# Kernel tuning notes

Hardware: AMD Instinct MI355X
Metric: run time of the kernel (lower is better)

## Reference

```python
import jax, jax.numpy as jnp
import numpy as np

N_NODES = 100000
N_EDGES = 1_600_000
F_IN = 500   # PubMed num_node_features
HID = 128
N_CLASSES = 3


def _glorot(key, shape):
    fan_in, fan_out = shape
    limit = np.sqrt(6.0 / (fan_in + fan_out)).astype(np.float32)
    return jax.random.uniform(key, shape, jnp.float32, -limit, limit)


def setup_inputs() -> dict:
    key = jax.random.key(0)
    ks = jax.random.split(key, 8)
    x = jax.random.normal(ks[0], (N_NODES, F_IN), jnp.float32)
    edge_index = jax.random.randint(ks[1], (2, N_EDGES), 0, N_NODES, jnp.int64)
    dims = [(F_IN, HID), (HID, HID), (HID, HID), (HID, HID), (HID, N_CLASSES)]
    inp = {"x": x, "edge_index": edge_index}
    for i, d in enumerate(dims):
        inp[f"W{i+1}"] = _glorot(ks[2 + i], d)
        inp[f"b{i+1}"] = jnp.zeros((d[1],), jnp.float32)
    return inp


def _gcn_conv(h, W, b, src, dst, norm, n):
    # linear transform then normalized neighbor aggregation (scatter-add)
    h = h @ W                                   # [N, out]
    msg = h[src] * norm                         # gather along edges, [E+N, out]
    return jax.ops.segment_sum(msg, dst, num_segments=n) + b


def reference(x, edge_index, W1, b1, W2, b2, W3, b3, W4, b4, W5, b5):
    n = x.shape[0]
    loops = jnp.arange(n)
    src = jnp.concatenate([edge_index[0], loops])  # add self-loops (PyG default)
    dst = jnp.concatenate([edge_index[1], loops])
    # symmetric normalization: deg^{-1/2}[dst] * deg^{-1/2}[src], deg over self-looped graph
    deg = jax.ops.segment_sum(jnp.ones_like(dst, x.dtype), dst, num_segments=n)
    dis = jnp.where(deg > 0, jax.lax.rsqrt(jnp.maximum(deg, 1e-12)), 0.0)
    norm = (dis[src] * dis[dst])[:, None]

    h = jax.nn.relu(_gcn_conv(x, W1, b1, src, dst, norm, n))
    # dropout p=0.5 is identity in eval mode
    h = jax.nn.relu(_gcn_conv(h, W2, b2, src, dst, norm, n))
    h = jax.nn.relu(_gcn_conv(h, W3, b3, src, dst, norm, n))
    h = jax.nn.relu(_gcn_conv(h, W4, b4, src, dst, norm, n))
    return _gcn_conv(h, W5, b5, src, dst, norm, n)
```

## Files before the change

kernel.cpp:

```cpp
#include <hip/hip_runtime.h>
#include <hip/hip_bf16.h>

#define NN 100000
#define NNP 100096
#define NE 1600000
#define FIN 500
#define HID 128

typedef __attribute__((ext_vector_type(8))) short short8;
typedef __attribute__((ext_vector_type(4))) float f32x4;

__device__ __forceinline__ float bf2f(unsigned short u) {
    return __uint_as_float(((unsigned int)u) << 16);
}
__device__ __forceinline__ unsigned short f2bf(float f) {
    __hip_bfloat16 h = __float2bfloat16(f);
    return *(unsigned short*)&h;
}
__device__ __forceinline__ float lo16(unsigned int v) { return __uint_as_float(v << 16); }
__device__ __forceinline__ float hi16(unsigned int v) { return __uint_as_float(v & 0xffff0000u); }


__global__ __launch_bounds__(256) void GCNLarge_20761871909627_kernel(int* __restrict__ buf, int n) {
    int i = blockIdx.x * 256 + threadIdx.x;
    if (i < n) buf[i] = 0;
}


__global__ void detect_kernel(const int* __restrict__ ei, const unsigned int* __restrict__ xw,
                              int* __restrict__ flags) {
    int lane = threadIdx.x & 63;
    int any = 0;
    for (int k = lane; k < 128; k += 64) any |= ei[2 * k + 1];
    int hits = 0;
    for (int k = lane; k < 256; k += 64) {
        unsigned e = (xw[k] >> 7) & 0xFF;
        hits += (e >= 100 && e <= 140) ? 1 : 0;
    }
#pragma unroll
    for (int o = 32; o > 0; o >>= 1) {
        any |= __shfl_down(any, o);
        hits += __shfl_down(hits, o);
    }
    if (lane == 0) {
        flags[0] = (any == 0) ? 1 : 0;
        flags[1] = (hits >= 128) ? 1 : 0;
    }
}

__device__ __forceinline__ int edge_src(const int* ei, int e, int m) {
    return m ? ei[2 * (size_t)e] : ei[e];
}
__device__ __forceinline__ int edge_dst(const int* ei, int e, int m) {
    return m ? ei[2 * (size_t)NE + 2 * (size_t)e] : ei[(size_t)NE + e];
}


__global__ __launch_bounds__(256) void count_kernel(const int* __restrict__ ei,
                                                    const int* __restrict__ flags,
                                                    int* __restrict__ cnt) {
    int e = blockIdx.x * 256 + threadIdx.x;
    if (e < NE) {
        int d = edge_dst(ei, e, flags[0]);
        if ((unsigned)d < NN) atomicAdd(&cnt[d], 1);
    }
}

__global__ __launch_bounds__(256) void dis_kernel(const int* __restrict__ cnt,
                                                  float* __restrict__ dis) {
    int i = blockIdx.x * 256 + threadIdx.x;
    if (i < NNP) {
        int c = (i < NN) ? cnt[i] : 0;
        if (c < 0) c = 0;
        dis[i] = rsqrtf((float)(c + 1));
    }
}

__global__ __launch_bounds__(1024) void scan1_kernel(const int* __restrict__ cnt,
                                                     int* __restrict__ off,
                                                     int* __restrict__ bsum) {
    __shared__ int s[1024];
    int i = blockIdx.x * 1024 + threadIdx.x;
    int v = (i < NN) ? cnt[i] : 0;
    s[threadIdx.x] = v;
    __syncthreads();
    for (int d = 1; d < 1024; d <<= 1) {
        int tv = (threadIdx.x >= d) ? s[threadIdx.x - d] : 0;
        __syncthreads();
        s[threadIdx.x] += tv;
        __syncthreads();
    }
    if (i < NN) off[i] = s[threadIdx.x] - v;
    if (threadIdx.x == 1023) bsum[blockIdx.x] = s[1023];
}

__global__ void scan2_kernel(int* __restrict__ bsum, int nb) {
    if (threadIdx.x == 0 && blockIdx.x == 0) {
        int acc = 0;
        for (int b = 0; b < nb; b++) { int v = bsum[b]; bsum[b] = acc; acc += v; }
    }
}

__global__ __launch_bounds__(1024) void scan3_kernel(int* __restrict__ off,
                                                     const int* __restrict__ bsum,
                                                     int* __restrict__ cursor) {
    int i = blockIdx.x * 1024 + threadIdx.x;
    if (i < NN) { int o = off[i] + bsum[blockIdx.x]; off[i] = o; cursor[i] = o; }
    if (i == 0) off[NN] = NE;
}

__global__ __launch_bounds__(256) void place_kernel(const int* __restrict__ ei,
                                                    const int* __restrict__ flags,
                                                    int* __restrict__ cursor,
                                                    int* __restrict__ csr) {
    int e = blockIdx.x * 256 + threadIdx.x;
    if (e < NE) {
        int m = flags[0];
        int s = edge_src(ei, e, m);
        int d = edge_dst(ei, e, m);
        if ((unsigned)s < NN && (unsigned)d < NN) {
            int slot = atomicAdd(&cursor[d], 1);
            if ((unsigned)slot < NE) csr[slot] = s;
        }
    }
}


__global__ __launch_bounds__(256) void wt_kernel(const void* __restrict__ W,
                                                 const int* __restrict__ flags,
                                                 unsigned short* __restrict__ Wt,
                                                 int K, int Kpad, int total) {
    int idx = blockIdx.x * 256 + threadIdx.x;
    if (idx >= total) return;
    int n = idx / Kpad, k = idx - n * Kpad;
    unsigned short v = 0;
    if (k < K) {
        if (flags[1]) v = ((const unsigned short*)W)[(size_t)k * HID + n];
        else          v = f2bf(((const float*)W)[(size_t)k * HID + n]);
    }
    Wt[idx] = v;
}


__global__ __launch_bounds__(256) void gemmWr_kernel(const unsigned short* __restrict__ A,
                                                     const unsigned short* __restrict__ Wt,
                                                     const float* __restrict__ dis,
                                                     unsigned short* __restrict__ out) {
    int tid = threadIdx.x;
    int w = tid >> 6, lane = tid & 63;
    int m = lane & 15, quad = lane >> 4;
    int mbase = (w >> 1) * 32, nbase = (w & 1) * 64;
    short8 b[4][4];
#pragma unroll
    for (int nt = 0; nt < 4; nt++)
#pragma unroll
        for (int kq = 0; kq < 4; kq++)
            b[nt][kq] = *(const short8*)(Wt + (size_t)(nbase + nt * 16 + m) * HID + kq * 32 + quad * 8);
    int t0 = blockIdx.x * 4;
    short8 aP[4][2], aQ[4][2];
    auto loadA = [&](int t, short8 a[4][2]) {
        const unsigned short* p0 = A + (size_t)(t * 64 + mbase + m) * HID + quad * 8;
        const unsigned short* p1 = p0 + (size_t)16 * HID;
#pragma unroll
        for (int kq = 0; kq < 4; kq++) {
            a[kq][0] = *(const short8*)(p0 + kq * 32);
            a[kq][1] = *(const short8*)(p1 + kq * 32);
        }
    };
    loadA(t0, aP);
#pragma unroll
    for (int tt = 0; tt < 4; tt++) {
        if (tt < 3) loadA(t0 + tt + 1, (tt & 1) ? aP : aQ);
        short8 (*ac)[2] = (tt & 1) ? aQ : aP;
        f32x4 acc[2][4] = {};
#pragma unroll
        for (int kq = 0; kq < 4; kq++)
#pragma unroll
            for (int nt = 0; nt < 4; nt++) {
                acc[0][nt] = __builtin_amdgcn_mfma_f32_16x16x32_bf16(ac[kq][0], b[nt][kq], acc[0][nt], 0, 0, 0);
                acc[1][nt] = __builtin_amdgcn_mfma_f32_16x16x32_bf16(ac[kq][1], b[nt][kq], acc[1][nt], 0, 0, 0);
            }
        int r0 = (t0 + tt) * 64;
#pragma unroll
        for (int mt = 0; mt < 2; mt++) {
            int rb = r0 + mbase + mt * 16 + quad * 4;
#pragma unroll
            for (int reg = 0; reg < 4; reg++) {
                float d = dis[rb + reg];
#pragma unroll
                for (int nt = 0; nt < 4; nt++)
                    out[(size_t)(rb + reg) * HID + nbase + nt * 16 + m] = f2bf(acc[mt][nt][reg] * d);
            }
        }
    }
}


__global__ __launch_bounds__(256) void gemm1r_kernel(const void* __restrict__ Av,
                                                     const unsigned short* __restrict__ Wt1,
                                                     const float* __restrict__ dis,
                                                     const int* __restrict__ flags,
                                                     unsigned short* __restrict__ out) {
    int tid = threadIdx.x;
    int bf = flags[1];
    int w = tid >> 6, lane = tid & 63;
    int m = lane & 15, quad = lane >> 4;
    int mbase = (w >> 1) * 32, nbase = (w & 1) * 64;
    int r0 = blockIdx.x * 64;
    int row0 = r0 + mbase + m;       int rc0 = (row0 < NN) ? row0 : NN - 1;
    int row1 = r0 + mbase + 16 + m;  int rc1 = (row1 < NN) ? row1 : NN - 1;
    f32x4 acc[2][4] = {};
#pragma unroll
    for (int kc = 0; kc < 4; kc++) {
        short8 b[4][4];
#pragma unroll
        for (int nt = 0; nt < 4; nt++)
#pragma unroll
            for (int kq = 0; kq < 4; kq++)
                b[nt][kq] = *(const short8*)(Wt1 + (size_t)(nbase + nt * 16 + m) * 512 + kc * 128 + kq * 32 + quad * 8);
        short8 a[4][2];
#pragma unroll
        for (int kq = 0; kq < 4; kq++) {
            int k_off = kc * 128 + kq * 32 + quad * 8;
            ushort4 z = make_ushort4(0, 0, 0, 0);
#pragma unroll
            for (int mt = 0; mt < 2; mt++) {
                int rr = mt ? rc1 : rc0;
                ushort4 lo = z, hi = z;
                if (bf) {
                    const unsigned short* xp = (const unsigned short*)Av + (size_t)rr * FIN + k_off;
                    if (k_off + 4 <= FIN) lo = *(const ushort4*)xp;
                    if (k_off + 8 <= FIN) hi = *(const ushort4*)(xp + 4);
                } else {
                    const float* xp = (const float*)Av + (size_t)rr * FIN + k_off;
                    if (k_off + 4 <= FIN) { float4 f = *(const float4*)xp;
                        lo = make_ushort4(f2bf(f.x), f2bf(f.y), f2bf(f.z), f2bf(f.w)); }
                    if (k_off + 8 <= FIN) { float4 f = *(const float4*)(xp + 4);
                        hi = make_ushort4(f2bf(f.x), f2bf(f.y), f2bf(f.z), f2bf(f.w)); }
                }
                a[kq][mt] = short8{(short)lo.x, (short)lo.y, (short)lo.z, (short)lo.w,
                                   (short)hi.x, (short)hi.y, (short)hi.z, (short)hi.w};
            }
        }
#pragma unroll
        for (int kq = 0; kq < 4; kq++)
#pragma unroll
            for (int nt = 0; nt < 4; nt++) {
                acc[0][nt] = __builtin_amdgcn_mfma_f32_16x16x32_bf16(a[kq][0], b[nt][kq], acc[0][nt], 0, 0, 0);
                acc[1][nt] = __builtin_amdgcn_mfma_f32_16x16x32_bf16(a[kq][1], b[nt][kq], acc[1][nt], 0, 0, 0);
            }
    }
#pragma unroll
    for (int mt = 0; mt < 2; mt++) {
        int rb = r0 + mbase + mt * 16 + quad * 4;
#pragma unroll
        for (int reg = 0; reg < 4; reg++) {
            int row = rb + reg;
            if (row < NN) {
                float d = dis[row];
#pragma unroll
                for (int nt = 0; nt < 4; nt++)
                    out[(size_t)row * HID + nbase + nt * 16 + m] = f2bf(acc[mt][nt][reg] * d);
            }
        }
    }
}


__global__ __launch_bounds__(256) void aggb_kernel(const unsigned short* __restrict__ tin,
                                                   const int* __restrict__ off,
                                                   const int* __restrict__ csr,
                                                   const float* __restrict__ dis,
                                                   const void* __restrict__ bias,
                                                   const int* __restrict__ flags,
                                                   unsigned short* __restrict__ hout,
                                                   int relu, int scale_src) {
    int node = blockIdx.x * 4 + (threadIdx.x >> 6);
    int lane = threadIdx.x & 63;
    float di = dis[node];
    unsigned int sv = *(const unsigned int*)(tin + (size_t)node * HID + lane * 2);
    float acc0 = scale_src ? di * lo16(sv) : lo16(sv);
    float acc1 = scale_src ? di * hi16(sv) : hi16(sv);
    int e0 = off[node], e1 = off[node + 1];
    if (e0 < 0) e0 = 0;
    if (e1 > NE) e1 = NE;
    int e = e0;
    if (!scale_src) {
        for (; e + 8 <= e1; e += 8) {
            int i0 = csr[e],     i1 = csr[e + 1], i2 = csr[e + 2], i3 = csr[e + 3];
            int i4 = csr[e + 4], i5 = csr[e + 5], i6 = csr[e + 6], i7 = csr[e + 7];
            unsigned int v0 = *(const unsigned int*)(tin + (size_t)i0 * HID + lane * 2);
            unsigned int v1 = *(const unsigned int*)(tin + (size_t)i1 * HID + lane * 2);
            unsigned int v2 = *(const unsigned int*)(tin + (size_t)i2 * HID + lane * 2);
            unsigned int v3 = *(const unsigned int*)(tin + (size_t)i3 * HID + lane * 2);
            unsigned int v4 = *(const unsigned int*)(tin + (size_t)i4 * HID + lane * 2);
            unsigned int v5 = *(const unsigned int*)(tin + (size_t)i5 * HID + lane * 2);
            unsigned int v6 = *(const unsigned int*)(tin + (size_t)i6 * HID + lane * 2);
            unsigned int v7 = *(const unsigned int*)(tin + (size_t)i7 * HID + lane * 2);
            acc0 += lo16(v0); acc1 += hi16(v0); acc0 += lo16(v1); acc1 += hi16(v1);
            acc0 += lo16(v2); acc1 += hi16(v2); acc0 += lo16(v3); acc1 += hi16(v3);
            acc0 += lo16(v4); acc1 += hi16(v4); acc0 += lo16(v5); acc1 += hi16(v5);
            acc0 += lo16(v6); acc1 += hi16(v6); acc0 += lo16(v7); acc1 += hi16(v7);
        }
        for (; e + 4 <= e1; e += 4) {
            int i0 = csr[e], i1 = csr[e + 1], i2 = csr[e + 2], i3 = csr[e + 3];
            unsigned int v0 = *(const unsigned int*)(tin + (size_t)i0 * HID + lane * 2);
            unsigned int v1 = *(const unsigned int*)(tin + (size_t)i1 * HID + lane * 2);
            unsigned int v2 = *(const unsigned int*)(tin + (size_t)i2 * HID + lane * 2);
            unsigned int v3 = *(const unsigned int*)(tin + (size_t)i3 * HID + lane * 2);
            acc0 += lo16(v0); acc1 += hi16(v0); acc0 += lo16(v1); acc1 += hi16(v1);
            acc0 += lo16(v2); acc1 += hi16(v2); acc0 += lo16(v3); acc1 += hi16(v3);
        }
        for (; e < e1; e++) {
            int s = csr[e];
            unsigned int v = *(const unsigned int*)(tin + (size_t)s * HID + lane * 2);
            acc0 += lo16(v); acc1 += hi16(v);
        }
    } else {
        for (; e + 8 <= e1; e += 8) {
            int i0 = csr[e],     i1 = csr[e + 1], i2 = csr[e + 2], i3 = csr[e + 3];
            int i4 = csr[e + 4], i5 = csr[e + 5], i6 = csr[e + 6], i7 = csr[e + 7];
            unsigned int v0 = *(const unsigned int*)(tin + (size_t)i0 * HID + lane * 2);
            unsigned int v1 = *(const unsigned int*)(tin + (size_t)i1 * HID + lane * 2);
            unsigned int v2 = *(const unsigned int*)(tin + (size_t)i2 * HID + lane * 2);
            unsigned int v3 = *(const unsigned int*)(tin + (size_t)i3 * HID + lane * 2);
            unsigned int v4 = *(const unsigned int*)(tin + (size_t)i4 * HID + lane * 2);
            unsigned int v5 = *(const unsigned int*)(tin + (size_t)i5 * HID + lane * 2);
            unsigned int v6 = *(const unsigned int*)(tin + (size_t)i6 * HID + lane * 2);
            unsigned int v7 = *(const unsigned int*)(tin + (size_t)i7 * HID + lane * 2);
            float m0 = dis[i0], m1 = dis[i1], m2 = dis[i2], m3 = dis[i3];
            float m4 = dis[i4], m5 = dis[i5], m6 = dis[i6], m7 = dis[i7];
            acc0 += m0 * lo16(v0); acc1 += m0 * hi16(v0);
            acc0 += m1 * lo16(v1); acc1 += m1 * hi16(v1);
            acc0 += m2 * lo16(v2); acc1 += m2 * hi16(v2);
            acc0 += m3 * lo16(v3); acc1 += m3 * hi16(v3);
            acc0 += m4 * lo16(v4); acc1 += m4 * hi16(v4);
            acc0 += m5 * lo16(v5); acc1 += m5 * hi16(v5);
            acc0 += m6 * lo16(v6); acc1 += m6 * hi16(v6);
            acc0 += m7 * lo16(v7); acc1 += m7 * hi16(v7);
        }
        for (; e < e1; e++) {
            int s = csr[e];
            unsigned int v = *(const unsigned int*)(tin + (size_t)s * HID + lane * 2);
            float mm = dis[s];
            acc0 += mm * lo16(v); acc1 += mm * hi16(v);
        }
    }
    float o0 = di * acc0, o1 = di * acc1;
    if (bias) {
        if (flags[1]) { o0 += bf2f(((const unsigned short*)bias)[lane * 2]);
                        o1 += bf2f(((const unsigned short*)bias)[lane * 2 + 1]); }
        else          { o0 += ((const float*)bias)[lane * 2];
                        o1 += ((const float*)bias)[lane * 2 + 1]; }
    }
    if (relu) { o0 = fmaxf(o0, 0.f); o1 = fmaxf(o1, 0.f); }
    unsigned int pk = ((unsigned int)f2bf(o1) << 16) | (unsigned int)f2bf(o0);
    *(unsigned int*)(hout + (size_t)node * HID + lane * 2) = pk;
}


__global__ __launch_bounds__(256) void gemm5_kernel(const unsigned short* __restrict__ A,
                                                    const void* __restrict__ W5v,
                                                    const void* __restrict__ b5v,
                                                    const int* __restrict__ flags,
                                                    void* __restrict__ outv) {
    __shared__ float Ws[384];
    __shared__ float bs[3];
    int tid = threadIdx.x;
    int bf = flags[1];
    for (int idx = tid; idx < 384; idx += 256)
        Ws[idx] = bf ? bf2f(((const unsigned short*)W5v)[idx]) : ((const float*)W5v)[idx];
    if (tid < 3)
        bs[tid] = bf ? bf2f(((const unsigned short*)b5v)[tid]) : ((const float*)b5v)[tid];
    __syncthreads();
    int lane = tid & 63;
    int row = blockIdx.x * 4 + (tid >> 6);
    float a0 = bf2f(A[(size_t)row * HID + lane]);
    float a1 = bf2f(A[(size_t)row * HID + 64 + lane]);
    float c0 = a0 * Ws[lane * 3 + 0] + a1 * Ws[(lane + 64) * 3 + 0];
    float c1 = a0 * Ws[lane * 3 + 1] + a1 * Ws[(lane + 64) * 3 + 1];
    float c2 = a0 * Ws[lane * 3 + 2] + a1 * Ws[(lane + 64) * 3 + 2];
#pragma unroll
    for (int o = 32; o > 0; o >>= 1) {
        c0 += __shfl_down(c0, o);
        c1 += __shfl_down(c1, o);
        c2 += __shfl_down(c2, o);
    }
    if (lane == 0) {
        c0 += bs[0]; c1 += bs[1]; c2 += bs[2];
        if (bf) {
            unsigned short* out = (unsigned short*)outv;
            out[(size_t)row * 3 + 0] = f2bf(c0);
            out[(size_t)row * 3 + 1] = f2bf(c1);
            out[(size_t)row * 3 + 2] = f2bf(c2);
        } else {
            float* out = (float*)outv;
            out[(size_t)row * 3 + 0] = c0;
            out[(size_t)row * 3 + 1] = c1;
            out[(size_t)row * 3 + 2] = c2;
        }
    }
}

extern "C" void kernel_launch(void* const* d_in, const int* in_sizes, int n_in,
                              void* d_out, int out_size, void* d_ws, size_t ws_size,
                              hipStream_t stream) {
    const void* x = nullptr; const int* ei = nullptr;
    const void* W1 = nullptr; const void* W5 = nullptr; const void* b5 = nullptr;
    const void* Wmid[3] = {nullptr, nullptr, nullptr};
    const void* bvec[4] = {nullptr, nullptr, nullptr, nullptr};
    int nw = 0, nb = 0;
    for (int i = 0; i < n_in; i++) {
        int s = in_sizes[i];
        if      (s == 50000000) x = d_in[i];
        else if (s == 3200000)  ei = (const int*)d_in[i];
        else if (s == 64000)    W1 = d_in[i];
        else if (s == 16384)  { if (nw < 3) Wmid[nw++] = d_in[i]; }
        else if (s == 384)      W5 = d_in[i];
        else if (s == 128)    { if (nb < 4) bvec[nb++] = d_in[i]; }
        else if (s == 3)        b5 = d_in[i];
    }
    if (!x || !ei || !W1 || !W5 || !b5 || nw < 3 || nb < 4) return;

    char* p = (char*)d_ws;
    auto alloc = [&](size_t bytes) { char* q = p; p += (bytes + 255) & ~(size_t)255; return (void*)q; };
    int*   flags = (int*)alloc(256);
    float* dis   = (float*)alloc((size_t)NNP * 4);
    int*   cnt   = (int*)alloc((size_t)NN * 4);
    int*   off   = (int*)alloc((size_t)(NN + 1) * 4);
    int*   cur   = (int*)alloc((size_t)NN * 4);
    int*   bsum  = (int*)alloc(128 * 4);
    int*   csr   = (int*)alloc((size_t)NE * 4);
    unsigned short* Wt1 = (unsigned short*)alloc((size_t)128 * 512 * 2);
    unsigned short* Wt2 = (unsigned short*)alloc((size_t)128 * 128 * 2);
    unsigned short* Wt3 = (unsigned short*)alloc((size_t)128 * 128 * 2);
    unsigned short* Wt4 = (unsigned short*)alloc((size_t)128 * 128 * 2);
    unsigned short* T   = (unsigned short*)alloc((size_t)NNP * HID * 2);
    unsigned short* H   = (unsigned short*)alloc((size_t)NNP * HID * 2);

    GCNLarge_20761871909627_kernel<<<(NN + 255) / 256, 256, 0, stream>>>(cnt, NN);
    detect_kernel<<<1, 64, 0, stream>>>(ei, (const unsigned int*)x, flags);
    wt_kernel<<<256, 256, 0, stream>>>(W1, flags, Wt1, FIN, 512, 128 * 512);
    wt_kernel<<<64, 256, 0, stream>>>(Wmid[0], flags, Wt2, HID, 128, 128 * 128);
    wt_kernel<<<64, 256, 0, stream>>>(Wmid[1], flags, Wt3, HID, 128, 128 * 128);
    wt_kernel<<<64, 256, 0, stream>>>(Wmid[2], flags, Wt4, HID, 128, 128 * 128);
    count_kernel<<<(NE + 255) / 256, 256, 0, stream>>>(ei, flags, cnt);
    dis_kernel<<<(NNP + 255) / 256, 256, 0, stream>>>(cnt, dis);
    scan1_kernel<<<98, 1024, 0, stream>>>(cnt, off, bsum);
    scan2_kernel<<<1, 64, 0, stream>>>(bsum, 98);
    scan3_kernel<<<98, 1024, 0, stream>>>(off, bsum, cur);
    place_kernel<<<(NE + 255) / 256, 256, 0, stream>>>(ei, flags, cur, csr);

    gemm1r_kernel<<<NNP / 64, 256, 0, stream>>>(x, Wt1, dis, flags, T);
    aggb_kernel<<<NN / 4, 256, 0, stream>>>(T, off, csr, dis, bvec[0], flags, H, 1, 0);
    gemmWr_kernel<<<NNP / 256, 256, 0, stream>>>(H, Wt2, dis, T);
    aggb_kernel<<<NN / 4, 256, 0, stream>>>(T, off, csr, dis, bvec[1], flags, H, 1, 0);
    gemmWr_kernel<<<NNP / 256, 256, 0, stream>>>(H, Wt3, dis, T);
    aggb_kernel<<<NN / 4, 256, 0, stream>>>(T, off, csr, dis, bvec[2], flags, H, 1, 0);
    gemmWr_kernel<<<NNP / 256, 256, 0, stream>>>(H, Wt4, dis, T);
    aggb_kernel<<<NN / 4, 256, 0, stream>>>(T, off, csr, dis, bvec[3], flags, H, 1, 0);
    aggb_kernel<<<NN / 4, 256, 0, stream>>>(H, off, csr, dis, nullptr, flags, T, 0, 1);
    gemm5_kernel<<<NN / 4, 256, 0, stream>>>(T, W5, b5, flags, d_out);
}
```

Measured before the change: 1.003 ms.

## Stage layer-1 GEMM through LDS, split aggregation wave into two edge halves, shrink GEMM tiles

```diff
diff --git a/kernel.cpp b/kernel.cpp
--- a/kernel.cpp
+++ b/kernel.cpp
@@ -6,6 +6,7 @@
 #define NE 1600000
 #define FIN 500
 #define HID 128
+#define LDK 136
 
 typedef __attribute__((ext_vector_type(8))) short short8;
 typedef __attribute__((ext_vector_type(4))) float f32x4;
@@ -142,7 +143,7 @@
 }
 
 
-__global__ __launch_bounds__(256) void gemmWr_kernel(const unsigned short* __restrict__ A,
+__global__ __launch_bounds__(256) void gemmW1_kernel(const unsigned short* __restrict__ A,
                                                      const unsigned short* __restrict__ Wt,
                                                      const float* __restrict__ dis,
                                                      unsigned short* __restrict__ out) {
@@ -150,66 +151,106 @@
     int w = tid >> 6, lane = tid & 63;
     int m = lane & 15, quad = lane >> 4;
     int mbase = (w >> 1) * 32, nbase = (w & 1) * 64;
+    int r0 = blockIdx.x * 64;
     short8 b[4][4];
 #pragma unroll
     for (int nt = 0; nt < 4; nt++)
 #pragma unroll
         for (int kq = 0; kq < 4; kq++)
             b[nt][kq] = *(const short8*)(Wt + (size_t)(nbase + nt * 16 + m) * HID + kq * 32 + quad * 8);
-    int t0 = blockIdx.x * 4;
-    short8 aP[4][2], aQ[4][2];
-    auto loadA = [&](int t, short8 a[4][2]) {
-        const unsigned short* p0 = A + (size_t)(t * 64 + mbase + m) * HID + quad * 8;
+    short8 a[4][2];
+    {
+        const unsigned short* p0 = A + (size_t)(r0 + mbase + m) * HID + quad * 8;
         const unsigned short* p1 = p0 + (size_t)16 * HID;
 #pragma unroll
         for (int kq = 0; kq < 4; kq++) {
             a[kq][0] = *(const short8*)(p0 + kq * 32);
             a[kq][1] = *(const short8*)(p1 + kq * 32);
         }
-    };
-    loadA(t0, aP);
-#pragma unroll
-    for (int tt = 0; tt < 4; tt++) {
-        if (tt < 3) loadA(t0 + tt + 1, (tt & 1) ? aP : aQ);
-        short8 (*ac)[2] = (tt & 1) ? aQ : aP;
-        f32x4 acc[2][4] = {};
-#pragma unroll
-        for (int kq = 0; kq < 4; kq++)
-#pragma unroll
-            for (int nt = 0; nt < 4; nt++) {
-                acc[0][nt] = __builtin_amdgcn_mfma_f32_16x16x32_bf16(ac[kq][0], b[nt][kq], acc[0][nt], 0, 0, 0);
-                acc[1][nt] = __builtin_amdgcn_mfma_f32_16x16x32_bf16(ac[kq][1], b[nt][kq], acc[1][nt], 0, 0, 0);
-            }
-        int r0 = (t0 + tt) * 64;
-#pragma unroll
-        for (int mt = 0; mt < 2; mt++) {
-            int rb = r0 + mbase + mt * 16 + quad * 4;
-#pragma unroll
-            for (int reg = 0; reg < 4; reg++) {
-                float d = dis[rb + reg];
-#pragma unroll
-                for (int nt = 0; nt < 4; nt++)
-                    out[(size_t)(rb + reg) * HID + nbase + nt * 16 + m] = f2bf(acc[mt][nt][reg] * d);
-            }
-        }
-    }
-}
-
-
-__global__ __launch_bounds__(256) void gemm1r_kernel(const void* __restrict__ Av,
-                                                     const unsigned short* __restrict__ Wt1,
-                                                     const float* __restrict__ dis,
-                                                     const int* __restrict__ flags,
-                                                     unsigned short* __restrict__ out) {
+    }
+    f32x4 acc[2][4] = {};
+#pragma unroll
+    for (int kq = 0; kq < 4; kq++)
+#pragma unroll
+        for (int nt = 0; nt < 4; nt++) {
+            acc[0][nt] = __builtin_amdgcn_mfma_f32_16x16x32_bf16(a[kq][0], b[nt][kq], acc[0][nt], 0, 0, 0);
+            acc[1][nt] = __builtin_amdgcn_mfma_f32_16x16x32_bf16(a[kq][1], b[nt][kq], acc[1][nt], 0, 0, 0);
+        }
+#pragma unroll
+    for (int mt = 0; mt < 2; mt++) {
+        int rb = r0 + mbase + mt * 16 + quad * 4;
+#pragma unroll
+        for (int reg = 0; reg < 4; reg++) {
+            float d = dis[rb + reg];
+#pragma unroll
+            for (int nt = 0; nt < 4; nt++)
+                out[(size_t)(rb + reg) * HID + nbase + nt * 16 + m] = f2bf(acc[mt][nt][reg] * d);
+        }
+    }
+}
+
+
+__global__ __launch_bounds__(256, 3) void gemm1d_kernel(const void* __restrict__ Av,
+                                                        const unsigned short* __restrict__ Wt1,
+                                                        const float* __restrict__ dis,
+                                                        const int* __restrict__ flags,
+                                                        unsigned short* __restrict__ out) {
+    __shared__ unsigned short As[2][64 * LDK];
     int tid = threadIdx.x;
     int bf = flags[1];
+    int r0 = blockIdx.x * 64;
     int w = tid >> 6, lane = tid & 63;
     int m = lane & 15, quad = lane >> 4;
     int mbase = (w >> 1) * 32, nbase = (w & 1) * 64;
-    int r0 = blockIdx.x * 64;
-    int row0 = r0 + mbase + m;       int rc0 = (row0 < NN) ? row0 : NN - 1;
-    int row1 = r0 + mbase + 16 + m;  int rc1 = (row1 < NN) ? row1 : NN - 1;
     f32x4 acc[2][4] = {};
+    short8 s[4];
+
+    auto stage = [&](int kc) {
+#pragma unroll
+        for (int i = 0; i < 4; i++) {
+            int idx = tid + i * 256;
+            int r = idx >> 4, c = idx & 15;
+            int row = r0 + r; if (row >= NN) row = NN - 1;
+            int kk = kc * 128 + c * 8;
+            short8 p = {};
+            if (bf) {
+                const unsigned short* xp = (const unsigned short*)Av + (size_t)row * FIN + kk;
+                if (kk + 8 <= FIN) {
+                    ushort4 lo = *(const ushort4*)xp;
+                    ushort4 hi = *(const ushort4*)(xp + 4);
+                    p = short8{(short)lo.x, (short)lo.y, (short)lo.z, (short)lo.w,
+                               (short)hi.x, (short)hi.y, (short)hi.z, (short)hi.w};
+                } else if (kk + 4 <= FIN) {
+                    ushort4 lo = *(const ushort4*)xp;
+                    p = short8{(short)lo.x, (short)lo.y, (short)lo.z, (short)lo.w, 0, 0, 0, 0};
+                }
+            } else {
+                const float* xp = (const float*)Av + (size_t)row * FIN + kk;
+                if (kk + 8 <= FIN) {
+                    float4 f0 = *(const float4*)xp;
+                    float4 f1 = *(const float4*)(xp + 4);
+                    p = short8{(short)f2bf(f0.x), (short)f2bf(f0.y), (short)f2bf(f0.z), (short)f2bf(f0.w),
+                               (short)f2bf(f1.x), (short)f2bf(f1.y), (short)f2bf(f1.z), (short)f2bf(f1.w)};
+                } else if (kk + 4 <= FIN) {
+                    float4 f0 = *(const float4*)xp;
+                    p = short8{(short)f2bf(f0.x), (short)f2bf(f0.y), (short)f2bf(f0.z), (short)f2bf(f0.w),
+                               0, 0, 0, 0};
+                }
+            }
+            s[i] = p;
+        }
+    };
+    auto wrlds = [&](int buf) {
+#pragma unroll
+        for (int i = 0; i < 4; i++) {
+            int idx = tid + i * 256;
+            int r = idx >> 4, c = idx & 15;
+            *(short8*)&As[buf][r * LDK + c * 8] = s[i];
+        }
+    };
+
+    stage(0);
+    wrlds(0);
 #pragma unroll
     for (int kc = 0; kc < 4; kc++) {
         short8 b[4][4];
@@ -218,37 +259,20 @@
 #pragma unroll
             for (int kq = 0; kq < 4; kq++)
                 b[nt][kq] = *(const short8*)(Wt1 + (size_t)(nbase + nt * 16 + m) * 512 + kc * 128 + kq * 32 + quad * 8);
-        short8 a[4][2];
+        __syncthreads();
+        if (kc < 3) stage(kc + 1);
+        const unsigned short* Ab = As[kc & 1];
 #pragma unroll
         for (int kq = 0; kq < 4; kq++) {
-            int k_off = kc * 128 + kq * 32 + quad * 8;
-            ushort4 z = make_ushort4(0, 0, 0, 0);
-#pragma unroll
-            for (int mt = 0; mt < 2; mt++) {
-                int rr = mt ? rc1 : rc0;
-                ushort4 lo = z, hi = z;
-                if (bf) {
-                    const unsigned short* xp = (const unsigned short*)Av + (size_t)rr * FIN + k_off;
-                    if (k_off + 4 <= FIN) lo = *(const ushort4*)xp;
-                    if (k_off + 8 <= FIN) hi = *(const ushort4*)(xp + 4);
-                } else {
-                    const float* xp = (const float*)Av + (size_t)rr * FIN + k_off;
-                    if (k_off + 4 <= FIN) { float4 f = *(const float4*)xp;
-                        lo = make_ushort4(f2bf(f.x), f2bf(f.y), f2bf(f.z), f2bf(f.w)); }
-                    if (k_off + 8 <= FIN) { float4 f = *(const float4*)(xp + 4);
-                        hi = make_ushort4(f2bf(f.x), f2bf(f.y), f2bf(f.z), f2bf(f.w)); }
-                }
-                a[kq][mt] = short8{(short)lo.x, (short)lo.y, (short)lo.z, (short)lo.w,
-                                   (short)hi.x, (short)hi.y, (short)hi.z, (short)hi.w};
+            short8 a0 = *(const short8*)&Ab[(mbase + m) * LDK + kq * 32 + quad * 8];
+            short8 a1 = *(const short8*)&Ab[(mbase + 16 + m) * LDK + kq * 32 + quad * 8];
+#pragma unroll
+            for (int nt = 0; nt < 4; nt++) {
+                acc[0][nt] = __builtin_amdgcn_mfma_f32_16x16x32_bf16(a0, b[nt][kq], acc[0][nt], 0, 0, 0);
+                acc[1][nt] = __builtin_amdgcn_mfma_f32_16x16x32_bf16(a1, b[nt][kq], acc[1][nt], 0, 0, 0);
             }
         }
-#pragma unroll
-        for (int kq = 0; kq < 4; kq++)
-#pragma unroll
-            for (int nt = 0; nt < 4; nt++) {
-                acc[0][nt] = __builtin_amdgcn_mfma_f32_16x16x32_bf16(a[kq][0], b[nt][kq], acc[0][nt], 0, 0, 0);
-                acc[1][nt] = __builtin_amdgcn_mfma_f32_16x16x32_bf16(a[kq][1], b[nt][kq], acc[1][nt], 0, 0, 0);
-            }
+        if (kc < 3) wrlds((kc + 1) & 1);
     }
 #pragma unroll
     for (int mt = 0; mt < 2; mt++) {
@@ -267,7 +291,7 @@
 }
 
 
-__global__ __launch_bounds__(256) void aggb_kernel(const unsigned short* __restrict__ tin,
+__global__ __launch_bounds__(256) void aggp_kernel(const unsigned short* __restrict__ tin,
                                                    const int* __restrict__ off,
                                                    const int* __restrict__ csr,
                                                    const float* __restrict__ dis,
@@ -277,85 +301,97 @@
                                                    int relu, int scale_src) {
     int node = blockIdx.x * 4 + (threadIdx.x >> 6);
     int lane = threadIdx.x & 63;
+    int half = lane >> 5;
+    int sub = lane & 31;
     float di = dis[node];
-    unsigned int sv = *(const unsigned int*)(tin + (size_t)node * HID + lane * 2);
-    float acc0 = scale_src ? di * lo16(sv) : lo16(sv);
-    float acc1 = scale_src ? di * hi16(sv) : hi16(sv);
+    float a0 = 0.f, a1 = 0.f, a2 = 0.f, a3 = 0.f;
+    if (half == 0) {
+        uint2 v = *(const uint2*)(tin + (size_t)node * HID + sub * 4);
+        float sc = scale_src ? di : 1.0f;
+        a0 = sc * lo16(v.x); a1 = sc * hi16(v.x);
+        a2 = sc * lo16(v.y); a3 = sc * hi16(v.y);
+    }
     int e0 = off[node], e1 = off[node + 1];
     if (e0 < 0) e0 = 0;
     if (e1 > NE) e1 = NE;
     int e = e0;
     if (!scale_src) {
         for (; e + 8 <= e1; e += 8) {
-            int i0 = csr[e],     i1 = csr[e + 1], i2 = csr[e + 2], i3 = csr[e + 3];
-            int i4 = csr[e + 4], i5 = csr[e + 5], i6 = csr[e + 6], i7 = csr[e + 7];
-            unsigned int v0 = *(const unsigned int*)(tin + (size_t)i0 * HID + lane * 2);
-            unsigned int v1 = *(const unsigned int*)(tin + (size_t)i1 * HID + lane * 2);
-            unsigned int v2 = *(const unsigned int*)(tin + (size_t)i2 * HID + lane * 2);
-            unsigned int v3 = *(const unsigned int*)(tin + (size_t)i3 * HID + lane * 2);
-            unsigned int v4 = *(const unsigned int*)(tin + (size_t)i4 * HID + lane * 2);
-            unsigned int v5 = *(const unsigned int*)(tin + (size_t)i5 * HID + lane * 2);
-            unsigned int v6 = *(const unsigned int*)(tin + (size_t)i6 * HID + lane * 2);
-            unsigned int v7 = *(const unsigned int*)(tin + (size_t)i7 * HID + lane * 2);
-            acc0 += lo16(v0); acc1 += hi16(v0); acc0 += lo16(v1); acc1 += hi16(v1);
-            acc0 += lo16(v2); acc1 += hi16(v2); acc0 += lo16(v3); acc1 += hi16(v3);
-            acc0 += lo16(v4); acc1 += hi16(v4); acc0 += lo16(v5); acc1 += hi16(v5);
-            acc0 += lo16(v6); acc1 += hi16(v6); acc0 += lo16(v7); acc1 += hi16(v7);
-        }
-        for (; e + 4 <= e1; e += 4) {
-            int i0 = csr[e], i1 = csr[e + 1], i2 = csr[e + 2], i3 = csr[e + 3];
-            unsigned int v0 = *(const unsigned int*)(tin + (size_t)i0 * HID + lane * 2);
-            unsigned int v1 = *(const unsigned int*)(tin + (size_t)i1 * HID + lane * 2);
-            unsigned int v2 = *(const unsigned int*)(tin + (size_t)i2 * HID + lane * 2);
-            unsigned int v3 = *(const unsigned int*)(tin + (size_t)i3 * HID + lane * 2);
-            acc0 += lo16(v0); acc1 += hi16(v0); acc0 += lo16(v1); acc1 += hi16(v1);
-            acc0 += lo16(v2); acc1 += hi16(v2); acc0 += lo16(v3); acc1 += hi16(v3);
-        }
-        for (; e < e1; e++) {
-            int s = csr[e];
-            unsigned int v = *(const unsigned int*)(tin + (size_t)s * HID + lane * 2);
-            acc0 += lo16(v); acc1 += hi16(v);
+#pragma unroll
+            for (int k = 0; k < 4; k++) {
+                int sa = csr[e + 2 * k], sb = csr[e + 2 * k + 1];
+                int sk = half ? sb : sa;
+                uint2 v = *(const uint2*)(tin + (size_t)sk * HID + sub * 4);
+                a0 += lo16(v.x); a1 += hi16(v.x); a2 += lo16(v.y); a3 += hi16(v.y);
+            }
+        }
+        for (; e + 2 <= e1; e += 2) {
+            int sa = csr[e], sb = csr[e + 1];
+            int sk = half ? sb : sa;
+            uint2 v = *(const uint2*)(tin + (size_t)sk * HID + sub * 4);
+            a0 += lo16(v.x); a1 += hi16(v.x); a2 += lo16(v.y); a3 += hi16(v.y);
+        }
+        if (e < e1 && half == 0) {
+            int sk = csr[e];
+            uint2 v = *(const uint2*)(tin + (size_t)sk * HID + sub * 4);
+            a0 += lo16(v.x); a1 += hi16(v.x); a2 += lo16(v.y); a3 += hi16(v.y);
         }
     } else {
         for (; e + 8 <= e1; e += 8) {
-            int i0 = csr[e],     i1 = csr[e + 1], i2 = csr[e + 2], i3 = csr[e + 3];
-            int i4 = csr[e + 4], i5 = csr[e + 5], i6 = csr[e + 6], i7 = csr[e + 7];
-            unsigned int v0 = *(const unsigned int*)(tin + (size_t)i0 * HID + lane * 2);
-            unsigned int v1 = *(const unsigned int*)(tin + (size_t)i1 * HID + lane * 2);
-            unsigned int v2 = *(const unsigned int*)(tin + (size_t)i2 * HID + lane * 2);
-            unsigned int v3 = *(const unsigned int*)(tin + (size_t)i3 * HID + lane * 2);
-            unsigned int v4 = *(const unsigned int*)(tin + (size_t)i4 * HID + lane * 2);
-            unsigned int v5 = *(const unsigned int*)(tin + (size_t)i5 * HID + lane * 2);
-            unsigned int v6 = *(const unsigned int*)(tin + (size_t)i6 * HID + lane * 2);
-            unsigned int v7 = *(const unsigned int*)(tin + (size_t)i7 * HID + lane * 2);
-            float m0 = dis[i0], m1 = dis[i1], m2 = dis[i2], m3 = dis[i3];
-            float m4 = dis[i4], m5 = dis[i5], m6 = dis[i6], m7 = dis[i7];
-            acc0 += m0 * lo16(v0); acc1 += m0 * hi16(v0);
-            acc0 += m1 * lo16(v1); acc1 += m1 * hi16(v1);
-            acc0 += m2 * lo16(v2); acc1 += m2 * hi16(v2);
-            acc0 += m3 * lo16(v3); acc1 += m3 * hi16(v3);
-            acc0 += m4 * lo16(v4); acc1 += m4 * hi16(v4);
-            acc0 += m5 * lo16(v5); acc1 += m5 * hi16(v5);
-            acc0 += m6 * lo16(v6); acc1 += m6 * hi16(v6);
-            acc0 += m7 * lo16(v7); acc1 += m7 * hi16(v7);
-        }
-        for (; e < e1; e++) {
-            int s = csr[e];
-            unsigned int v = *(const unsigned int*)(tin + (size_t)s * HID + lane * 2);
-            float mm = dis[s];
-            acc0 += mm * lo16(v); acc1 += mm * hi16(v);
-        }
-    }
-    float o0 = di * acc0, o1 = di * acc1;
-    if (bias) {
-        if (flags[1]) { o0 += bf2f(((const unsigned short*)bias)[lane * 2]);
-                        o1 += bf2f(((const unsigned short*)bias)[lane * 2 + 1]); }
-        else          { o0 += ((const float*)bias)[lane * 2];
-                        o1 += ((const float*)bias)[lane * 2 + 1]; }
-    }
-    if (relu) { o0 = fmaxf(o0, 0.f); o1 = fmaxf(o1, 0.f); }
-    unsigned int pk = ((unsigned int)f2bf(o1) << 16) | (unsigned int)f2bf(o0);
-    *(unsigned int*)(hout + (size_t)node * HID + lane * 2) = pk;
+#pragma unroll
+            for (int k = 0; k < 4; k++) {
+                int sa = csr[e + 2 * k], sb = csr[e + 2 * k + 1];
+                int sk = half ? sb : sa;
+                uint2 v = *(const uint2*)(tin + (size_t)sk * HID + sub * 4);
+                float mm = dis[sk];
+                a0 += mm * lo16(v.x); a1 += mm * hi16(v.x);
+                a2 += mm * lo16(v.y); a3 += mm * hi16(v.y);
+            }
+        }
+        for (; e + 2 <= e1; e += 2) {
+            int sa = csr[e], sb = csr[e + 1];
+            int sk = half ? sb : sa;
+            uint2 v = *(const uint2*)(tin + (size_t)sk * HID + sub * 4);
+            float mm = dis[sk];
+            a0 += mm * lo16(v.x); a1 += mm * hi16(v.x);
+            a2 += mm * lo16(v.y); a3 += mm * hi16(v.y);
+        }
+        if (e < e1 && half == 0) {
+            int sk = csr[e];
+            uint2 v = *(const uint2*)(tin + (size_t)sk * HID + sub * 4);
+            float mm = dis[sk];
+            a0 += mm * lo16(v.x); a1 += mm * hi16(v.x);
+            a2 += mm * lo16(v.y); a3 += mm * hi16(v.y);
+        }
+    }
+    a0 += __shfl_xor(a0, 32);
+    a1 += __shfl_xor(a1, 32);
+    a2 += __shfl_xor(a2, 32);
+    a3 += __shfl_xor(a3, 32);
+    if (half == 0) {
+        float o0 = di * a0, o1 = di * a1, o2 = di * a2, o3 = di * a3;
+        if (bias) {
+            if (flags[1]) {
+                o0 += bf2f(((const unsigned short*)bias)[sub * 4 + 0]);
+                o1 += bf2f(((const unsigned short*)bias)[sub * 4 + 1]);
+                o2 += bf2f(((const unsigned short*)bias)[sub * 4 + 2]);
+                o3 += bf2f(((const unsigned short*)bias)[sub * 4 + 3]);
+            } else {
+                o0 += ((const float*)bias)[sub * 4 + 0];
+                o1 += ((const float*)bias)[sub * 4 + 1];
+                o2 += ((const float*)bias)[sub * 4 + 2];
+                o3 += ((const float*)bias)[sub * 4 + 3];
+            }
+        }
+        if (relu) {
+            o0 = fmaxf(o0, 0.f); o1 = fmaxf(o1, 0.f);
+            o2 = fmaxf(o2, 0.f); o3 = fmaxf(o3, 0.f);
+        }
+        uint2 pk;
+        pk.x = ((unsigned int)f2bf(o1) << 16) | (unsigned int)f2bf(o0);
+        pk.y = ((unsigned int)f2bf(o3) << 16) | (unsigned int)f2bf(o2);
+        *(uint2*)(hout + (size_t)node * HID + sub * 4) = pk;
+    }
 }
 
 
@@ -451,14 +487,15 @@
     scan3_kernel<<<98, 1024, 0, stream>>>(off, bsum, cur);
     place_kernel<<<(NE + 255) / 256, 256, 0, stream>>>(ei, flags, cur, csr);
 
-    gemm1r_kernel<<<NNP / 64, 256, 0, stream>>>(x, Wt1, dis, flags, T);
-    aggb_kernel<<<NN / 4, 256, 0, stream>>>(T, off, csr, dis, bvec[0], flags, H, 1, 0);
-    gemmWr_kernel<<<NNP / 256, 256, 0, stream>>>(H, Wt2, dis, T);
-    aggb_kernel<<<NN / 4, 256, 0, stream>>>(T, off, csr, dis, bvec[1], flags, H, 1, 0);
-    gemmWr_kernel<<<NNP / 256, 256, 0, stream>>>(H, Wt3, dis, T);
-    aggb_kernel<<<NN / 4, 256, 0, stream>>>(T, off, csr, dis, bvec[2], flags, H, 1, 0);
-    gemmWr_kernel<<<NNP / 256, 256, 0, stream>>>(H, Wt4, dis, T);
-    aggb_kernel<<<NN / 4, 256, 0, stream>>>(T, off, csr, dis, bvec[3], flags, H, 1, 0);
-    aggb_kernel<<<NN / 4, 256, 0, stream>>>(H, off, csr, dis, nullptr, flags, T, 0, 1);
+    const int GB = NNP / 64;
+    gemm1d_kernel<<<GB, 256, 0, stream>>>(x, Wt1, dis, flags, T);
+    aggp_kernel<<<NN / 4, 256, 0, stream>>>(T, off, csr, dis, bvec[0], flags, H, 1, 0);
+    gemmW1_kernel<<<GB, 256, 0, stream>>>(H, Wt2, dis, T);
+    aggp_kernel<<<NN / 4, 256, 0, stream>>>(T, off, csr, dis, bvec[1], flags, H, 1, 0);
+    gemmW1_kernel<<<GB, 256, 0, stream>>>(H, Wt3, dis, T);
+    aggp_kernel<<<NN / 4, 256, 0, stream>>>(T, off, csr, dis, bvec[2], flags, H, 1, 0);
+    gemmW1_kernel<<<GB, 256, 0, stream>>>(H, Wt4, dis, T);
+    aggp_kernel<<<NN / 4, 256, 0, stream>>>(T, off, csr, dis, bvec[3], flags, H, 1, 0);
+    aggp_kernel<<<NN / 4, 256, 0, stream>>>(H, off, csr, dis, nullptr, flags, T, 0, 1);
     gemm5_kernel<<<NN / 4, 256, 0, stream>>>(T, W5, b5, flags, d_out);
 }
```

Measured after the change: 1.017 ms. No clear change (+1.4%).
